# Performance work log

Measured on AMD Instinct MI355X. Metric: run time of the kernel, lower is better.

## Reference

```python
import jax, jax.numpy as jnp
import numpy as np
import math

EARTH_RADIUS_KM = 6371.0
D_MAX_KM = 200.0
K_D = 64

B, N, D, R = 64, 128, 128, 4096


def setup_inputs() -> dict:
    key = jax.random.key(0)
    ks = jax.random.split(key, 7)
    S = jax.random.normal(ks[0], (B, N, D), dtype=jnp.float32)
    region_emb = jax.random.normal(ks[1], (R, D), dtype=jnp.float32)
    traj_lat = jax.random.uniform(ks[2], (B, N), dtype=jnp.float32)
    traj_lon = jax.random.uniform(ks[3], (B, N), dtype=jnp.float32)
    region_centroids = jax.random.uniform(ks[4], (R, 2), dtype=jnp.float32)
    key_padding_mask = jax.random.randint(ks[5], (B, N), 0, 2).astype(bool)
    E_d_match = jax.random.normal(ks[6], (K_D,), dtype=jnp.float32) * 0.1
    return {"S": S, "region_emb": region_emb, "traj_lat": traj_lat,
            "traj_lon": traj_lon, "region_centroids": region_centroids,
            "key_padding_mask": key_padding_mask, "E_d_match": E_d_match}


def _haversine_km(lat1, lon1, lat2, lon2):
    deg2rad = math.pi / 180.0
    lat1r = lat1 * deg2rad
    lat2r = lat2 * deg2rad
    dlat = (lat2 - lat1) * deg2rad
    dlon = (lon2 - lon1) * deg2rad
    a = jnp.sin(dlat / 2) ** 2 + jnp.cos(lat1r) * jnp.cos(lat2r) * jnp.sin(dlon / 2) ** 2
    a = jnp.clip(a, 0.0, 1.0)
    return EARTH_RADIUS_KM * 2.0 * jnp.arcsin(jnp.sqrt(a))


def _interp_scalar(table, x):
    K = table.shape[0]
    x = jnp.clip(x, 0.0, K - 1 - 1e-06)
    k = jnp.floor(x).astype(jnp.int32)
    frac = x - k.astype(x.dtype)
    lo = table[k]
    hi = table[jnp.minimum(k + 1, K - 1)]
    return (1.0 - frac) * lo + frac * hi


def reference(S, region_emb, traj_lat, traj_lon, region_centroids,
              key_padding_mask, E_d_match):
    Dm = S.shape[-1]
    cand_lat = region_centroids[:, 0]  # [R]
    cand_lon = region_centroids[:, 1]
    # [B, n, R] pairwise distance trajectory-position <-> region centroid
    dd = _haversine_km(traj_lat[:, :, None], traj_lon[:, :, None],
                       cand_lat[None, None, :], cand_lon[None, None, :])
    d_bin = jnp.clip(dd, 0.0, D_MAX_KM) / D_MAX_KM * (K_D - 1)
    bias_match = _interp_scalar(E_d_match, d_bin)  # [B, n, R]
    scores = jnp.einsum('bnd,rd->bnr', S, region_emb) / math.sqrt(Dm)
    scores = scores + bias_match
    mask = key_padding_mask[:, :, None]  # [B, n, 1]
    scores = jnp.where(mask, -jnp.inf, scores)
    attn = jnp.nan_to_num(jax.nn.softmax(scores, axis=1), nan=0.0)
    scores_safe = jnp.where(mask, 0.0, scores)
    return (attn * scores_safe).sum(axis=1)  # [B, R]
```

## Files before the change

kernel.cpp:

```cpp
#include <hip/hip_runtime.h>
#include <math.h>

#define BB 64
#define NN 128
#define DD 128
#define RR 4096
#define KD 64

typedef _Float16 f16x8 __attribute__((ext_vector_type(8)));
typedef float    float4v __attribute__((ext_vector_type(4)));

__global__ __launch_bounds__(256, 4)
void matching_kernel(const float* __restrict__ S,
                     const float* __restrict__ Remb,
                     const float* __restrict__ tlat,
                     const float* __restrict__ tlon,
                     const float* __restrict__ cent,
                     const int*   __restrict__ kpm,
                     const float* __restrict__ Etab,
                     float* __restrict__ out)
{
    __shared__ _Float16 ldsE[128 * 128];
    __shared__ float colLatP[128], colLonP[128], colCos[128];
    __shared__ float rowLatP[128], rowLonP[128], rowCn[128];
    __shared__ float2 tab2[KD];
    __shared__ float pe[4][128], pw[4][128];

    const int tid = threadIdx.x;
    const int b  = blockIdx.y;
    const int r0 = blockIdx.x * 128;

    const float D2R   = 0.017453292519943295f;
    const float HD2R  = 0.008726646259971648f;
    const float SCALE = 0.08838834764831845f;
    const float XMUL  = 12742.0f * 0.315f;

    if (tid < 128) {
        int r = r0 + tid;
        float cla = cent[2 * r], clo = cent[2 * r + 1];
        colLatP[tid] = cla * HD2R; colLonP[tid] = clo * HD2R;
        colCos[tid]  = cosf(cla * D2R);
    } else {
        int n = tid - 128;
        float la = tlat[b * NN + n], lo = tlon[b * NN + n];
        rowLatP[n] = la * HD2R; rowLonP[n] = lo * HD2R;
        float cn = cosf(la * D2R);
        rowCn[n] = (kpm[b * NN + n] != 0) ? -cn : cn;
    }
    if (tid < KD) {
        float lo = Etab[tid];
        float hi = Etab[tid < KD - 1 ? tid + 1 : KD - 1];
        tab2[tid] = make_float2(lo, hi - lo);
    }

    const float* gE = Remb + (size_t)r0 * DD;
    for (int i = tid; i < 128 * 16; i += 256) {
        int row = i >> 4, c = i & 15;
        const float* p = &gE[row * DD + c * 8];
        float4 lo = *(const float4*)p, hi = *(const float4*)(p + 4);
        f16x8 h;
        h[0] = (_Float16)lo.x; h[1] = (_Float16)lo.y;
        h[2] = (_Float16)lo.z; h[3] = (_Float16)lo.w;
        h[4] = (_Float16)hi.x; h[5] = (_Float16)hi.y;
        h[6] = (_Float16)hi.z; h[7] = (_Float16)hi.w;
        *(f16x8*)&ldsE[row * 128 + ((c ^ (row & 15)) * 8)] = h;
    }
    __syncthreads();

    const int wv = tid >> 6, lane = tid & 63;
    const int lrow = lane & 15, quad = lane >> 4;

    const float* gS = S + (size_t)b * NN * DD;
    f16x8 afrag[2][4];
#pragma unroll
    for (int i = 0; i < 2; ++i) {
        const float* rp = &gS[((2 * wv + i) * 16 + lrow) * DD];
#pragma unroll
        for (int kk = 0; kk < 4; ++kk) {
            float4 lo = *(const float4*)&rp[kk * 32 + quad * 8];
            float4 hi = *(const float4*)&rp[kk * 32 + quad * 8 + 4];
            f16x8 a;
            a[0] = (_Float16)lo.x; a[1] = (_Float16)lo.y;
            a[2] = (_Float16)lo.z; a[3] = (_Float16)lo.w;
            a[4] = (_Float16)hi.x; a[5] = (_Float16)hi.y;
            a[6] = (_Float16)hi.z; a[7] = (_Float16)hi.w;
            afrag[i][kk] = a;
        }
    }

    float4v acc[2][8] = {};
#pragma unroll
    for (int kk = 0; kk < 4; ++kk) {
#pragma unroll
        for (int tr = 0; tr < 8; ++tr) {
            int c = kk * 4 + quad;
            f16x8 bb = *(const f16x8*)&ldsE[(tr * 16 + lrow) * 128 + ((c ^ lrow) * 8)];
            acc[0][tr] = __builtin_amdgcn_mfma_f32_16x16x32_f16(afrag[0][kk], bb, acc[0][tr], 0, 0, 0);
            acc[1][tr] = __builtin_amdgcn_mfma_f32_16x16x32_f16(afrag[1][kk], bb, acc[1][tr], 0, 0, 0);
        }
    }

    float tlP[8], toP[8], cn8[8];
#pragma unroll
    for (int i = 0; i < 2; ++i)
#pragma unroll
        for (int e = 0; e < 4; ++e) {
            int n = (2 * wv + i) * 16 + quad * 4 + e;
            int j = i * 4 + e;
            tlP[j] = rowLatP[n]; toP[j] = rowLonP[n]; cn8[j] = rowCn[n];
        }

#pragma unroll
    for (int tr = 0; tr < 8; ++tr) {
        int col = tr * 16 + lrow;
        float claP = colLatP[col], cloP = colLonP[col], cc = colCos[col];
        float es = 0.0f, ws = 0.0f;
#pragma unroll
        for (int i = 0; i < 2; ++i)
#pragma unroll
            for (int e = 0; e < 4; ++e) {
                int j = i * 4 + e;
                float hd = claP - tlP[j];
                float ho = cloP - toP[j];
                float a  = fmaf(hd, hd, (cn8[j] * cc) * (ho * ho));
                float sq = sqrtf(a);
                float as = sq * fmaf(a, 0.16666667f, 1.0f);
                float x  = fminf(as * XMUL, 62.999996f);
                int   k  = (int)x;
                float fr = x - (float)k;
                float2 te = tab2[k];
                float bias = fmaf(fr, te.y, te.x);
                float s  = fmaf(acc[i][tr][e], SCALE, bias);
                float ex = __expf(s);
                ex = (cn8[j] < 0.0f) ? 0.0f : ex;
                es += ex;
                ws = fmaf(ex, s, ws);
            }
        es += __shfl_xor(es, 16, 64); es += __shfl_xor(es, 32, 64);
        ws += __shfl_xor(ws, 16, 64); ws += __shfl_xor(ws, 32, 64);
        if (lane < 16) { pe[wv][col] = es; pw[wv][col] = ws; }
    }
    __syncthreads();

    if (tid < 128) {
        float es = pe[0][tid] + pe[1][tid] + pe[2][tid] + pe[3][tid];
        float ws = pw[0][tid] + pw[1][tid] + pw[2][tid] + pw[3][tid];
        float o = es > 0.0f ? ws / es : 0.0f;
        out[(size_t)b * RR + r0 + tid] = o;
    }
}

extern "C" void kernel_launch(void* const* d_in, const int* in_sizes, int n_in,
                              void* d_out, int out_size, void* d_ws, size_t ws_size,
                              hipStream_t stream) {
    const float* S    = (const float*)d_in[0];
    const float* Remb = (const float*)d_in[1];
    const float* tlat = (const float*)d_in[2];
    const float* tlon = (const float*)d_in[3];
    const float* cent = (const float*)d_in[4];
    const int*   kpm  = (const int*)d_in[5];
    const float* Etab = (const float*)d_in[6];
    float* out = (float*)d_out;

    dim3 grid(RR / 128, BB, 1);
    dim3 block(256, 1, 1);
    matching_kernel<<<grid, block, 0, stream>>>(S, Remb, tlat, tlon, cent, kpm, Etab, out);
}
```

Baseline: 110.0 us.

## Compact unmasked rows and skip MFMA/epilogue work for padded positions

Builds a ballot-based compaction of the unmasked trajectory positions per batch, gathers only those rows of S, and skips MFMA tiles and bias/softmax epilogue work for 16-row tiles that hold only padding. It also switches to exp2 with constants pre-scaled by log2(e), replaces the arcsin polynomial with a single sqrt of a scaled argument, and reuses the embedding LDS buffer for the partial sums. The aim is to cut the matrix-multiply and transcendental work roughly in proportion to the masked fraction, at the cost of an extra barrier, the gather, and divergent per-wave tile counts. Dropping the cubic arcsin term changes the distance approximation for larger distances.

```diff
diff --git a/kernel.cpp b/kernel.cpp
--- a/kernel.cpp
+++ b/kernel.cpp
@@ -24,35 +24,39 @@
     __shared__ float colLatP[128], colLonP[128], colCos[128];
     __shared__ float rowLatP[128], rowLonP[128], rowCn[128];
     __shared__ float2 tab2[KD];
-    __shared__ float pe[4][128], pw[4][128];
+    __shared__ int   idx[128];
+    __shared__ unsigned long long smask[2];
+
+    float* pe = (float*)ldsE;
+    float* pw = (float*)ldsE + 512;
 
     const int tid = threadIdx.x;
     const int b  = blockIdx.y;
     const int r0 = blockIdx.x * 128;
-
-    const float D2R   = 0.017453292519943295f;
-    const float HD2R  = 0.008726646259971648f;
-    const float SCALE = 0.08838834764831845f;
-    const float XMUL  = 12742.0f * 0.315f;
+    const int wv = tid >> 6, lane = tid & 63;
+    const int lrow = lane & 15, quad = lane >> 4;
+
+    const float D2R    = 0.017453292519943295f;
+    const float HD2R   = 0.008726646259971648f;
+    const float L2E    = 1.4426950408889634f;
+    const float SCALE2 = 0.08838834764831845f * 1.4426950408889634f;
+    const float XMSQ   = 4013.73f * 4013.73f;
+    const float LN2    = 0.6931471805599453f;
 
     if (tid < 128) {
         int r = r0 + tid;
         float cla = cent[2 * r], clo = cent[2 * r + 1];
         colLatP[tid] = cla * HD2R; colLonP[tid] = clo * HD2R;
         colCos[tid]  = cosf(cla * D2R);
-    } else {
-        int n = tid - 128;
-        float la = tlat[b * NN + n], lo = tlon[b * NN + n];
-        rowLatP[n] = la * HD2R; rowLonP[n] = lo * HD2R;
-        float cn = cosf(la * D2R);
-        rowCn[n] = (kpm[b * NN + n] != 0) ? -cn : cn;
-    }
-    if (tid < KD) {
-        float lo = Etab[tid];
-        float hi = Etab[tid < KD - 1 ? tid + 1 : KD - 1];
-        tab2[tid] = make_float2(lo, hi - lo);
-    }
-
+        bool valid = (kpm[b * NN + tid] == 0);
+        unsigned long long m = __ballot(valid);
+        if (lane == 0) smask[wv] = m;
+    } else if (tid < 128 + KD) {
+        int k = tid - 128;
+        float lo = Etab[k];
+        float hi = Etab[k < KD - 1 ? k + 1 : KD - 1];
+        tab2[k] = make_float2(lo * L2E, (hi - lo) * L2E);
+    }
     const float* gE = Remb + (size_t)r0 * DD;
     for (int i = tid; i < 128 * 16; i += 256) {
         int row = i >> 4, c = i & 15;
@@ -67,45 +71,78 @@
     }
     __syncthreads();
 
-    const int wv = tid >> 6, lane = tid & 63;
-    const int lrow = lane & 15, quad = lane >> 4;
+    const unsigned long long m0 = smask[0], m1 = smask[1];
+    const int c0 = __popcll(m0);
+    const int V  = c0 + __popcll(m1);
+    const int Mt = (V + 15) >> 4;
+
+    if (tid < 128) {
+        unsigned long long mw = (tid < 64) ? m0 : m1;
+        int ln = tid & 63;
+        if ((mw >> ln) & 1ull) {
+            int pos = __popcll(mw & ((1ull << ln) - 1ull)) + (tid < 64 ? 0 : c0);
+            idx[pos] = tid;
+        }
+    }
+    __syncthreads();
+
+    if (tid < 128) {
+        if (tid < V) {
+            int n = idx[tid];
+            float la = tlat[b * NN + n], lo = tlon[b * NN + n];
+            rowLatP[tid] = la * HD2R; rowLonP[tid] = lo * HD2R;
+            rowCn[tid]   = cosf(la * D2R);
+        } else {
+            rowLatP[tid] = 0.0f; rowLonP[tid] = 0.0f; rowCn[tid] = -1.0f;
+        }
+    }
 
     const float* gS = S + (size_t)b * NN * DD;
+    const bool a1 = (wv + 4) < Mt;
     f16x8 afrag[2][4];
 #pragma unroll
     for (int i = 0; i < 2; ++i) {
-        const float* rp = &gS[((2 * wv + i) * 16 + lrow) * DD];
+        int tile = wv + 4 * i;
+        if (tile < Mt) {
+            int rc = tile * 16 + lrow;
+            int n  = idx[rc < V ? rc : V - 1];
+            const float* rp = &gS[n * DD];
+#pragma unroll
+            for (int kk = 0; kk < 4; ++kk) {
+                float4 lo = *(const float4*)&rp[kk * 32 + quad * 8];
+                float4 hi = *(const float4*)&rp[kk * 32 + quad * 8 + 4];
+                f16x8 a;
+                a[0] = (_Float16)lo.x; a[1] = (_Float16)lo.y;
+                a[2] = (_Float16)lo.z; a[3] = (_Float16)lo.w;
+                a[4] = (_Float16)hi.x; a[5] = (_Float16)hi.y;
+                a[6] = (_Float16)hi.z; a[7] = (_Float16)hi.w;
+                afrag[i][kk] = a;
+            }
+        }
+    }
+
+    float4v acc[2][8] = {};
+    if (wv < Mt) {
 #pragma unroll
         for (int kk = 0; kk < 4; ++kk) {
-            float4 lo = *(const float4*)&rp[kk * 32 + quad * 8];
-            float4 hi = *(const float4*)&rp[kk * 32 + quad * 8 + 4];
-            f16x8 a;
-            a[0] = (_Float16)lo.x; a[1] = (_Float16)lo.y;
-            a[2] = (_Float16)lo.z; a[3] = (_Float16)lo.w;
-            a[4] = (_Float16)hi.x; a[5] = (_Float16)hi.y;
-            a[6] = (_Float16)hi.z; a[7] = (_Float16)hi.w;
-            afrag[i][kk] = a;
-        }
-    }
-
-    float4v acc[2][8] = {};
-#pragma unroll
-    for (int kk = 0; kk < 4; ++kk) {
-#pragma unroll
-        for (int tr = 0; tr < 8; ++tr) {
-            int c = kk * 4 + quad;
-            f16x8 bb = *(const f16x8*)&ldsE[(tr * 16 + lrow) * 128 + ((c ^ lrow) * 8)];
-            acc[0][tr] = __builtin_amdgcn_mfma_f32_16x16x32_f16(afrag[0][kk], bb, acc[0][tr], 0, 0, 0);
-            acc[1][tr] = __builtin_amdgcn_mfma_f32_16x16x32_f16(afrag[1][kk], bb, acc[1][tr], 0, 0, 0);
-        }
-    }
+#pragma unroll
+            for (int tr = 0; tr < 8; ++tr) {
+                int c = kk * 4 + quad;
+                f16x8 bb = *(const f16x8*)&ldsE[(tr * 16 + lrow) * 128 + ((c ^ lrow) * 8)];
+                acc[0][tr] = __builtin_amdgcn_mfma_f32_16x16x32_f16(afrag[0][kk], bb, acc[0][tr], 0, 0, 0);
+                if (a1)
+                    acc[1][tr] = __builtin_amdgcn_mfma_f32_16x16x32_f16(afrag[1][kk], bb, acc[1][tr], 0, 0, 0);
+            }
+        }
+    }
+    __syncthreads();
 
     float tlP[8], toP[8], cn8[8];
 #pragma unroll
     for (int i = 0; i < 2; ++i)
 #pragma unroll
         for (int e = 0; e < 4; ++e) {
-            int n = (2 * wv + i) * 16 + quad * 4 + e;
+            int n = (wv + 4 * i) * 16 + quad * 4 + e;
             int j = i * 4 + e;
             tlP[j] = rowLatP[n]; toP[j] = rowLonP[n]; cn8[j] = rowCn[n];
         }
@@ -114,38 +151,40 @@
     for (int tr = 0; tr < 8; ++tr) {
         int col = tr * 16 + lrow;
         float claP = colLatP[col], cloP = colLonP[col], cc = colCos[col];
-        float es = 0.0f, ws = 0.0f;
-#pragma unroll
-        for (int i = 0; i < 2; ++i)
-#pragma unroll
-            for (int e = 0; e < 4; ++e) {
-                int j = i * 4 + e;
-                float hd = claP - tlP[j];
-                float ho = cloP - toP[j];
-                float a  = fmaf(hd, hd, (cn8[j] * cc) * (ho * ho));
-                float sq = sqrtf(a);
-                float as = sq * fmaf(a, 0.16666667f, 1.0f);
-                float x  = fminf(as * XMUL, 62.999996f);
-                int   k  = (int)x;
-                float fr = x - (float)k;
-                float2 te = tab2[k];
-                float bias = fmaf(fr, te.y, te.x);
-                float s  = fmaf(acc[i][tr][e], SCALE, bias);
-                float ex = __expf(s);
-                ex = (cn8[j] < 0.0f) ? 0.0f : ex;
-                es += ex;
-                ws = fmaf(ex, s, ws);
+        float es = 0.0f, ws2 = 0.0f;
+        if (wv < Mt) {
+#pragma unroll
+            for (int i = 0; i < 2; ++i) {
+                if (i == 1 && !a1) break;
+#pragma unroll
+                for (int e = 0; e < 4; ++e) {
+                    int j = i * 4 + e;
+                    float hd = claP - tlP[j];
+                    float ho = cloP - toP[j];
+                    float a  = fmaf(hd, hd, (cn8[j] * cc) * (ho * ho));
+                    float x  = fminf(__builtin_amdgcn_sqrtf(a * XMSQ), 62.999996f);
+                    int   k  = (int)x;
+                    float fr = x - (float)k;
+                    float2 te = tab2[k];
+                    float bias2 = fmaf(fr, te.y, te.x);
+                    float s2 = fmaf(acc[i][tr][e], SCALE2, bias2);
+                    float ex = __builtin_amdgcn_exp2f(s2);
+                    ex = (cn8[j] < 0.0f) ? 0.0f : ex;
+                    es += ex;
+                    ws2 = fmaf(ex, s2, ws2);
+                }
             }
-        es += __shfl_xor(es, 16, 64); es += __shfl_xor(es, 32, 64);
-        ws += __shfl_xor(ws, 16, 64); ws += __shfl_xor(ws, 32, 64);
-        if (lane < 16) { pe[wv][col] = es; pw[wv][col] = ws; }
-    }
-    __syncthreads();
-
-    if (tid < 128) {
-        float es = pe[0][tid] + pe[1][tid] + pe[2][tid] + pe[3][tid];
-        float ws = pw[0][tid] + pw[1][tid] + pw[2][tid] + pw[3][tid];
-        float o = es > 0.0f ? ws / es : 0.0f;
+        }
+        es  += __shfl_xor(es, 16, 64);  es  += __shfl_xor(es, 32, 64);
+        ws2 += __shfl_xor(ws2, 16, 64); ws2 += __shfl_xor(ws2, 32, 64);
+        if (lane < 16) { pe[wv * 128 + col] = es; pw[wv * 128 + col] = ws2; }
+    }
+    __syncthreads();
+
+    if (tid < 128) {
+        float es = pe[tid] + pe[128 + tid] + pe[256 + tid] + pe[384 + tid];
+        float ws = pw[tid] + pw[128 + tid] + pw[256 + tid] + pw[384 + tid];
+        float o = es > 0.0f ? (ws / es) * LN2 : 0.0f;
         out[(size_t)b * RR + r0 + tid] = o;
     }
 }
```

After: 96.26 us. 12.5% less time.
